# Kernel optimization log

Measured on AMD Instinct MI355X. Metric: run time of the kernel, lower is better.

## Reference

```python
import jax, jax.numpy as jnp
import numpy as np

B, S, D = 2, 1024, 768
H, HD = 12, 64
E, K, F = 8, 2, 3072
EPS = 1e-5


def _ln(x, g, b):
    mu = jnp.mean(x, -1, keepdims=True)
    var = jnp.mean(jnp.square(x - mu), -1, keepdims=True)
    return (x - mu) * jax.lax.rsqrt(var + EPS) * g + b


def setup_inputs() -> dict:
    key = jax.random.key(0)
    ks = jax.random.split(key, 12)
    s = lambda k, shape, sc: jax.random.normal(k, shape, jnp.float32) * sc
    return {
        "hidden_states": s(ks[0], (B, S, D), 1.0),
        "ln1_g": jnp.ones((D,), jnp.float32), "ln1_b": jnp.zeros((D,), jnp.float32),
        "w_attn": s(ks[1], (D, 3 * D), 0.02), "b_attn": jnp.zeros((3 * D,), jnp.float32),
        "w_attnproj": s(ks[2], (D, D), 0.02), "b_attnproj": jnp.zeros((D,), jnp.float32),
        "ln2_g": jnp.ones((D,), jnp.float32), "ln2_b": jnp.zeros((D,), jnp.float32),
        "w_router": s(ks[3], (E, D), 0.01),
        "w_fc": s(ks[4], (E, D, F), 0.02 / E), "b_fc": jnp.zeros((E, F), jnp.float32),
        "w_proj": s(ks[5], (E, F, D), 0.02 / E), "b_proj": jnp.zeros((E, D), jnp.float32),
    }


def reference(hidden_states, ln1_g, ln1_b, w_attn, b_attn, w_attnproj, b_attnproj,
              ln2_g, ln2_b, w_router, w_fc, b_fc, w_proj, b_proj):
    # --- attention sub-block (GPT-2 style, causal) ---
    residual = hidden_states
    x = _ln(hidden_states, ln1_g, ln1_b)
    qkv = x @ w_attn + b_attn                         # [B,S,3D]
    q, k, v = jnp.split(qkv, 3, axis=-1)
    def heads(t):
        return t.reshape(B, S, H, HD).transpose(0, 2, 1, 3)  # [B,H,S,HD]
    q, k, v = heads(q), heads(k), heads(v)
    scores = jnp.einsum("bhqd,bhkd->bhqk", q, k) / np.sqrt(HD).astype(np.float32)
    causal = jnp.tril(jnp.ones((S, S), bool))
    scores = jnp.where(causal, scores, jnp.finfo(scores.dtype).min)
    attn = jax.nn.softmax(scores, axis=-1)
    ctx = jnp.einsum("bhqk,bhkd->bhqd", attn, v)
    ctx = ctx.transpose(0, 2, 1, 3).reshape(B, S, D)
    attn_out = ctx @ w_attnproj + b_attnproj
    hs = attn_out + residual

    # --- MoE FFN sub-block ---
    residual = hs
    x2 = _ln(hs, ln2_g, ln2_b)
    logits = x2 @ w_router.T                          # [B,S,E]
    probs = jax.nn.softmax(logits, axis=-1)
    top_w, top_idx = jax.lax.top_k(probs, K)          # [B,S,K]
    top_w = top_w / jnp.sum(top_w, -1, keepdims=True)
    gates = jnp.sum(jax.nn.one_hot(top_idx, E, dtype=x2.dtype) * top_w[..., None], axis=2)  # [B,S,E]
    h = jax.nn.gelu(jnp.einsum("bsd,edf->bsef", x2, w_fc) + b_fc, approximate=False)
    y = jnp.einsum("bsef,efd->bsed", h, w_proj) + b_proj
    moe_out = jnp.einsum("bse,bsed->bsd", gates, y)
    return moe_out + residual
```

## Files before the change

### kernel.cpp

```cpp
#include <hip/hip_runtime.h>
#include <hip/hip_bf16.h>
#include <math.h>

#define NB 2
#define SEQ 1024
#define DM 768
#define NHEAD 12
#define HDIM 64
#define NEXP 8
#define FF 3072
#define NTOK (NB*SEQ)
#define TDIM (3*DM)
#define LNEPS 1e-5f
#define NSLOT (NTOK*2)

typedef __attribute__((ext_vector_type(8))) short v8s;
typedef __attribute__((ext_vector_type(4))) float v4f;

#define GLDS16(src, dst) \
    __builtin_amdgcn_global_load_lds((const __attribute__((address_space(1))) unsigned int*)(src), \
                                     (__attribute__((address_space(3))) unsigned int*)(dst), 16, 0, 0)

#define BARF() do { asm volatile("" ::: "memory"); __builtin_amdgcn_s_barrier(); asm volatile("" ::: "memory"); } while(0)
#define WAITV(n) asm volatile("s_waitcnt vmcnt(" #n ")" ::: "memory")

static __device__ __forceinline__ float bf2f(unsigned short u){
    return __uint_as_float(((unsigned)u) << 16);
}
static __device__ __forceinline__ unsigned short f2bf(float f){
    unsigned u = __float_as_uint(f);
    u += 0x7fffu + ((u >> 16) & 1u);
    return (unsigned short)(u >> 16);
}
static __device__ __forceinline__ float gelu_exact(float x){
    return 0.5f * x * (1.0f + erff(x * 0.70710678118654752440f));
}

__global__ __launch_bounds__(256) void tconv_kernel(const float* __restrict__ in,
                                                    unsigned short* __restrict__ out,
                                                    int R, int C){
    __shared__ float T[64][33];
    size_t base = (size_t)blockIdx.z * R * C;
    int c0 = blockIdx.x * 32, r0 = blockIdx.y * 64;
    int t = threadIdx.x;
    int row = t >> 2, cq = (t & 3) * 8;
    const float* ip = &in[base + (size_t)(r0 + row) * C + c0 + cq];
    float4 va = *(const float4*)ip;
    float4 vb = *(const float4*)(ip + 4);
    T[row][cq+0]=va.x; T[row][cq+1]=va.y; T[row][cq+2]=va.z; T[row][cq+3]=va.w;
    T[row][cq+4]=vb.x; T[row][cq+5]=vb.y; T[row][cq+6]=vb.z; T[row][cq+7]=vb.w;
    __syncthreads();
    int oc = t >> 3, or8 = (t & 7) * 8;
    unsigned short ov[8];
    #pragma unroll
    for (int i = 0; i < 8; i++) ov[i] = f2bf(T[or8 + i][oc]);
    *(v8s*)&out[base + (size_t)(c0 + oc) * R + r0 + or8] = *(const v8s*)ov;
}

__global__ __launch_bounds__(256) void ln_b(const float* __restrict__ in,
                                            const float* __restrict__ g,
                                            const float* __restrict__ b,
                                            unsigned short* __restrict__ outb){
    int t = blockIdx.x;
    const float* row = in + (size_t)t * DM;
    int tid = threadIdx.x;
    float v0 = row[tid], v1 = row[tid + 256], v2 = row[tid + 512];
    float s  = v0 + v1 + v2;
    float ss = v0*v0 + v1*v1 + v2*v2;
    for (int off = 32; off; off >>= 1){
        s  += __shfl_down(s, off);
        ss += __shfl_down(ss, off);
    }
    __shared__ float ls[4], lss[4];
    int wid = tid >> 6, lane = tid & 63;
    if (lane == 0){ ls[wid] = s; lss[wid] = ss; }
    __syncthreads();
    if (tid == 0){
        float a = ls[0] + ls[1] + ls[2] + ls[3];
        float c = lss[0] + lss[1] + lss[2] + lss[3];
        float mu = a / (float)DM;
        float var = c / (float)DM - mu * mu;
        ls[0] = mu; lss[0] = rsqrtf(var + LNEPS);
    }
    __syncthreads();
    float mu = ls[0], rs = lss[0];
    unsigned short* obrow = outb + (size_t)t * DM;
    obrow[tid]     = f2bf((v0 - mu) * rs * g[tid]       + b[tid]);
    obrow[tid+256] = f2bf((v1 - mu) * rs * g[tid + 256] + b[tid + 256]);
    obrow[tid+512] = f2bf((v2 - mu) * rs * g[tid + 512] + b[tid + 512]);
}

__global__ __launch_bounds__(256) void ln_router(const float* __restrict__ in,
                                                 const float* __restrict__ g,
                                                 const float* __restrict__ b,
                                                 const float* __restrict__ wr,
                                                 unsigned short* __restrict__ outb,
                                                 int* __restrict__ cnt,
                                                 int* __restrict__ expTok,
                                                 int* __restrict__ tokE,
                                                 int* __restrict__ tokPos,
                                                 float* __restrict__ tokGate){
    int t = blockIdx.x;
    const float* row = in + (size_t)t * DM;
    int tid = threadIdx.x;
    float v0 = row[tid], v1 = row[tid + 256], v2 = row[tid + 512];
    float s  = v0 + v1 + v2;
    float ss = v0*v0 + v1*v1 + v2*v2;
    for (int off = 32; off; off >>= 1){
        s  += __shfl_down(s, off);
        ss += __shfl_down(ss, off);
    }
    __shared__ float ls[4], lss[4];
    __shared__ float wsum[4][NEXP];
    int wid = tid >> 6, lane = tid & 63;
    if (lane == 0){ ls[wid] = s; lss[wid] = ss; }
    __syncthreads();
    if (tid == 0){
        float a = ls[0] + ls[1] + ls[2] + ls[3];
        float c = lss[0] + lss[1] + lss[2] + lss[3];
        float mu = a / (float)DM;
        float var = c / (float)DM - mu * mu;
        ls[0] = mu; lss[0] = rsqrtf(var + LNEPS);
    }
    __syncthreads();
    float mu = ls[0], rs = lss[0];
    float o0 = (v0 - mu) * rs * g[tid]       + b[tid];
    float o1 = (v1 - mu) * rs * g[tid + 256] + b[tid + 256];
    float o2 = (v2 - mu) * rs * g[tid + 512] + b[tid + 512];
    unsigned short* obrow = outb + (size_t)t * DM;
    obrow[tid] = f2bf(o0); obrow[tid+256] = f2bf(o1); obrow[tid+512] = f2bf(o2);
    float p[NEXP];
    #pragma unroll
    for (int e = 0; e < NEXP; e++)
        p[e] = o0*wr[e*DM + tid] + o1*wr[e*DM + tid + 256] + o2*wr[e*DM + tid + 512];
    #pragma unroll
    for (int e = 0; e < NEXP; e++)
        for (int off = 32; off; off >>= 1) p[e] += __shfl_down(p[e], off);
    if (lane == 0){
        #pragma unroll
        for (int e = 0; e < NEXP; e++) wsum[wid][e] = p[e];
    }
    __syncthreads();
    if (tid == 0){
        float lg[NEXP];
        #pragma unroll
        for (int e = 0; e < NEXP; e++)
            lg[e] = wsum[0][e] + wsum[1][e] + wsum[2][e] + wsum[3][e];
        int i0 = 0; float m0 = lg[0];
        #pragma unroll
        for (int e = 1; e < NEXP; e++) if (lg[e] > m0){ m0 = lg[e]; i0 = e; }
        int i1 = -1; float m1 = -INFINITY;
        #pragma unroll
        for (int e = 0; e < NEXP; e++) if (e != i0 && lg[e] > m1){ m1 = lg[e]; i1 = e; }
        float mx = fmaxf(m0, m1);
        float e0 = __expf(m0 - mx), e1 = __expf(m1 - mx);
        float inv = 1.0f / (e0 + e1);
        int p0 = atomicAdd(&cnt[i0], 1);
        int p1 = atomicAdd(&cnt[i1], 1);
        expTok[i0*NTOK + p0] = t;
        expTok[i1*NTOK + p1] = t;
        tokE[t*2]   = i0; tokE[t*2+1]   = i1;
        tokPos[t*2] = p0; tokPos[t*2+1] = p1;
        tokGate[t*2]   = e0 * inv;
        tokGate[t*2+1] = e1 * inv;
    }
}

__global__ __launch_bounds__(256) void mm_qkv(const unsigned short* __restrict__ Ab,
                                              const unsigned short* __restrict__ Bb,
                                              const float* __restrict__ bias,
                                              unsigned short* __restrict__ Qb,
                                              unsigned short* __restrict__ Kb,
                                              unsigned short* __restrict__ Vt){
    __shared__ __align__(16) unsigned short As[2][64*32];
    __shared__ __align__(16) unsigned short Bs[2][64*32];
    int bm = blockIdx.y * 64, bn = blockIdx.x * 64;
    int tid = threadIdx.x, wave = tid >> 6, lane = tid & 63;
    int quad = lane >> 4, l15 = lane & 15;
    int wm = wave >> 1, wn = wave & 1;
    int arow = tid >> 2, achunk = (tid & 3) * 8;
    const unsigned short* aS = Ab + (size_t)(bm + arow) * DM + achunk;
    const unsigned short* bS = Bb + (size_t)(bn + arow) * DM + achunk;
    v4f acc[2][2];
    #pragma unroll
    for (int i = 0; i < 2; i++)
        #pragma unroll
        for (int j = 0; j < 2; j++) acc[i][j] = (v4f){0.f,0.f,0.f,0.f};

#define QKV_STAGE(buf, kt) do { int kb = (kt)*32; \
    GLDS16(aS + kb, &As[buf][(wave*16)*32]); \
    GLDS16(bS + kb, &Bs[buf][(wave*16)*32]); \
} while(0)
#define QKV_COMP(buf) do { \
    v8s a[2], bfr[2]; \
    _Pragma("unroll") \
    for (int i = 0; i < 2; i++){ \
        a[i]   = *(const v8s*)&As[buf][(wm*32 + i*16 + l15)*32 + quad*8]; \
        bfr[i] = *(const v8s*)&Bs[buf][(wn*32 + i*16 + l15)*32 + quad*8]; \
    } \
    _Pragma("unroll") \
    for (int mi = 0; mi < 2; mi++) \
        _Pragma("unroll") \
        for (int ni = 0; ni < 2; ni++) \
            acc[mi][ni] = __builtin_amdgcn_mfma_f32_16x16x32_bf16(a[mi], bfr[ni], acc[mi][ni], 0, 0, 0); \
} while(0)

    const int NK = DM/32;
    QKV_STAGE(0, 0);
    #pragma unroll 1
    for (int kt = 0; kt < NK; kt++){
        if (NK - kt > 1){ QKV_STAGE((kt+1)&1, kt+1); WAITV(2); }
        else            { WAITV(0); }
        BARF();
        QKV_COMP(kt&1);
        BARF();
    }
    int btyp = bn / DM;
    #pragma unroll
    for (int ni = 0; ni < 2; ni++){
        int n = bn + wn*32 + ni*16 + l15;
        float bb = bias[n];
        int hd = n % DM; int h = hd >> 6; int d = hd & 63;
        #pragma unroll
        for (int mi = 0; mi < 2; mi++){
            int m = bm + wm*32 + mi*16 + quad*4;
            int b = m >> 10, sd = m & 1023;
            size_t bhbase = (size_t)(b*NHEAD + h);
            if (btyp == 0){
                #pragma unroll
                for (int r = 0; r < 4; r++)
                    Qb[(bhbase*SEQ + sd + r)*HDIM + d] = f2bf((acc[mi][ni][r] + bb) * 0.125f);
            } else if (btyp == 1){
                #pragma unroll
                for (int r = 0; r < 4; r++)
                    Kb[(bhbase*SEQ + sd + r)*HDIM + d] = f2bf(acc[mi][ni][r] + bb);
            } else {
                ushort4 o;
                o.x = f2bf(acc[mi][ni][0] + bb); o.y = f2bf(acc[mi][ni][1] + bb);
                o.z = f2bf(acc[mi][ni][2] + bb); o.w = f2bf(acc[mi][ni][3] + bb);
                *(ushort4*)&Vt[(bhbase*HDIM + d)*SEQ + sd] = o;
            }
        }
    }
}

__global__ __launch_bounds__(128) void fattn(const unsigned short* __restrict__ Qb,
                                             const unsigned short* __restrict__ Kb,
                                             const unsigned short* __restrict__ Vt,
                                             unsigned short* __restrict__ ctxb){
    int bh = blockIdx.x >> 5;
    int q0 = (31 - (blockIdx.x & 31)) * 32;
    int h = bh % NHEAD, b = bh / NHEAD;
    int wv = threadIdx.x >> 6;
    int lane = threadIdx.x & 63;
    int quad = lane >> 4, l15 = lane & 15;

    __shared__ __align__(16) unsigned short Plds[2][32*32];
    __shared__ __align__(16) v4f Oex[2][4][64];
    __shared__ float Mm[2][4][64];
    __shared__ float Lm[2][4][64];

    const unsigned short* qp = Qb + ((size_t)bh*SEQ + q0 + l15) * HDIM + quad*8;
    v8s qa00 = *(const v8s*)qp;
    v8s qa01 = *(const v8s*)(qp + 32);
    v8s qa10 = *(const v8s*)(qp + 16*HDIM);
    v8s qa11 = *(const v8s*)(qp + 16*HDIM + 32);

    v4f o[2][4];
    #pragma unroll
    for (int i = 0; i < 2; i++)
        #pragma unroll
        for (int j = 0; j < 4; j++) o[i][j] = (v4f){0.f,0.f,0.f,0.f};
    float mrow[2][4], lrow[2][4];
    #pragma unroll
    for (int i = 0; i < 2; i++)
        #pragma unroll
        for (int r = 0; r < 4; r++){ mrow[i][r] = -1e30f; lrow[i][r] = 0.f; }

    int nch = (q0 >> 5) + 1;
    int halfc = (nch + 1) >> 1;
    int ch0 = wv ? halfc : 0;
    int ch1 = wv ? nch : halfc;
    unsigned short* Pw = &Plds[wv][0];

    for (int ch = ch0; ch < ch1; ch++){
        int kt = ch * 32;
        const unsigned short* kp = Kb + ((size_t)bh*SEQ + kt + l15) * HDIM + quad*8;
        v8s k00 = *(const v8s*)kp;
        v8s k01 = *(const v8s*)(kp + 32);
        v8s k10 = *(const v8s*)(kp + 16*HDIM);
        v8s k11 = *(const v8s*)(kp + 16*HDIM + 32);
        v4f s00 = {0,0,0,0}, s01 = {0,0,0,0}, s10 = {0,0,0,0}, s11 = {0,0,0,0};
        s00 = __builtin_amdgcn_mfma_f32_16x16x32_bf16(qa00, k00, s00, 0, 0, 0);
        s00 = __builtin_amdgcn_mfma_f32_16x16x32_bf16(qa01, k01, s00, 0, 0, 0);
        s01 = __builtin_amdgcn_mfma_f32_16x16x32_bf16(qa00, k10, s01, 0, 0, 0);
        s01 = __builtin_amdgcn_mfma_f32_16x16x32_bf16(qa01, k11, s01, 0, 0, 0);
        s10 = __builtin_amdgcn_mfma_f32_16x16x32_bf16(qa10, k00, s10, 0, 0, 0);
        s10 = __builtin_amdgcn_mfma_f32_16x16x32_bf16(qa11, k01, s10, 0, 0, 0);
        s11 = __builtin_amdgcn_mfma_f32_16x16x32_bf16(qa10, k10, s11, 0, 0, 0);
        s11 = __builtin_amdgcn_mfma_f32_16x16x32_bf16(qa11, k11, s11, 0, 0, 0);

        int key0 = kt + l15, key1 = kt + 16 + l15;
        float alpha[2][4];
        #pragma unroll
        for (int mi = 0; mi < 2; mi++){
            #pragma unroll
            for (int r = 0; r < 4; r++){
                int qrow = q0 + mi*16 + quad*4 + r;
                float sv0 = mi ? s10[r] : s00[r];
                float sv1 = mi ? s11[r] : s01[r];
                float v0 = (key0 <= qrow) ? sv0 : -1e30f;
                float v1 = (key1 <= qrow) ? sv1 : -1e30f;
                float mx = fmaxf(v0, v1);
                mx = fmaxf(mx, __shfl_xor(mx, 1));
                mx = fmaxf(mx, __shfl_xor(mx, 2));
                mx = fmaxf(mx, __shfl_xor(mx, 4));
                mx = fmaxf(mx, __shfl_xor(mx, 8));
                float mn = fmaxf(mrow[mi][r], mx);
                alpha[mi][r] = __expf(mrow[mi][r] - mn);
                float p0 = __expf(v0 - mn);
                float p1 = __expf(v1 - mn);
                float ps = p0 + p1;
                ps += __shfl_xor(ps, 1);
                ps += __shfl_xor(ps, 2);
                ps += __shfl_xor(ps, 4);
                ps += __shfl_xor(ps, 8);
                lrow[mi][r] = lrow[mi][r] * alpha[mi][r] + ps;
                mrow[mi][r] = mn;
                Pw[(mi*16 + quad*4 + r)*32 + l15]      = f2bf(p0);
                Pw[(mi*16 + quad*4 + r)*32 + 16 + l15] = f2bf(p1);
            }
        }
        #pragma unroll
        for (int mi = 0; mi < 2; mi++)
            #pragma unroll
            for (int df = 0; df < 4; df++)
                #pragma unroll
                for (int r = 0; r < 4; r++)
                    o[mi][df][r] *= alpha[mi][r];
        v8s pa0 = *(const v8s*)&Pw[l15*32 + quad*8];
        v8s pa1 = *(const v8s*)&Pw[(16 + l15)*32 + quad*8];
        const unsigned short* vp = Vt + ((size_t)bh*HDIM + l15) * SEQ + kt + quad*8;
        #pragma unroll
        for (int df = 0; df < 4; df++){
            v8s vb = *(const v8s*)(vp + df*16*SEQ);
            o[0][df] = __builtin_amdgcn_mfma_f32_16x16x32_bf16(pa0, vb, o[0][df], 0, 0, 0);
            o[1][df] = __builtin_amdgcn_mfma_f32_16x16x32_bf16(pa1, vb, o[1][df], 0, 0, 0);
        }
    }

    int other = 1 - wv;
    #pragma unroll
    for (int df = 0; df < 4; df++) Oex[wv][df][lane] = o[other][df];
    #pragma unroll
    for (int r = 0; r < 4; r++){ Mm[wv][r][lane] = mrow[other][r]; Lm[wv][r][lane] = lrow[other][r]; }
    __syncthreads();
    v4f oth[4];
    #pragma unroll
    for (int df = 0; df < 4; df++) oth[df] = Oex[other][df][lane];
    #pragma unroll
    for (int r = 0; r < 4; r++){
        float mo = Mm[other][r][lane], lo_ = Lm[other][r][lane];
        float mm = mrow[wv][r], lm = lrow[wv][r];
        float M = fmaxf(mm, mo);
        float am = __expf(mm - M), ao = __expf(mo - M);
        float L = lm*am + lo_*ao;
        float inv = 1.0f / L;
        size_t orow = (size_t)(b*SEQ + q0 + wv*16 + quad*4 + r) * DM + h*HDIM;
        #pragma unroll
        for (int df = 0; df < 4; df++)
            ctxb[orow + df*16 + l15] = f2bf((o[wv][df][r]*am + oth[df][r]*ao) * inv);
    }
}

__global__ __launch_bounds__(256) void mm_attnproj(const unsigned short* __restrict__ Ab,
                                                   const unsigned short* __restrict__ Bb,
                                                   const float* __restrict__ bias,
                                                   const float* __restrict__ res,
                                                   float* __restrict__ C){
    __shared__ __align__(16) unsigned short As[4][64*32];
    __shared__ __align__(16) unsigned short Bs[4][64*32];
    int bm = blockIdx.y * 64, bn = blockIdx.x * 64;
    int tid = threadIdx.x, wave = tid >> 6, lane = tid & 63;
    int quad = lane >> 4, l15 = lane & 15;
    int wm = wave >> 1, wn = wave & 1;
    int lrow = lane >> 2, lchunk = (lane & 3) * 8;
    const unsigned short* aS = Ab + (size_t)(bm + wave*16 + lrow) * DM + lchunk;
    const unsigned short* bS = Bb + (size_t)(bn + wave*16 + lrow) * DM + lchunk;
    v4f acc[2][2];
    #pragma unroll
    for (int i = 0; i < 2; i++)
        #pragma unroll
        for (int j = 0; j < 2; j++) acc[i][j] = (v4f){0.f,0.f,0.f,0.f};

#define AP_STAGE(buf, kt) do { int kb = (kt)*32; \
    GLDS16(aS + kb, &As[buf][(wave*16)*32]); \
    GLDS16(bS + kb, &Bs[buf][(wave*16)*32]); \
} while(0)
#define AP_COMP(buf) do { \
    v8s a[2], bfr[2]; \
    _Pragma("unroll") \
    for (int i = 0; i < 2; i++){ \
        a[i]   = *(const v8s*)&As[buf][(wm*32 + i*16 + l15)*32 + quad*8]; \
        bfr[i] = *(const v8s*)&Bs[buf][(wn*32 + i*16 + l15)*32 + quad*8]; \
    } \
    _Pragma("unroll") \
    for (int mi = 0; mi < 2; mi++) \
        _Pragma("unroll") \
        for (int ni = 0; ni < 2; ni++) \
            acc[mi][ni] = __builtin_amdgcn_mfma_f32_16x16x32_bf16(a[mi], bfr[ni], acc[mi][ni], 0, 0, 0); \
} while(0)

    const int NK = DM/32;
    AP_STAGE(0, 0); AP_STAGE(1, 1); AP_STAGE(2, 2);
    #pragma unroll 1
    for (int kt = 0; kt < NK; kt++){
        int rem = NK - kt;
        if (rem > 3){ AP_STAGE((kt+3)&3, kt+3); WAITV(6); }
        else if (rem == 3){ WAITV(4); }
        else if (rem == 2){ WAITV(2); }
        else { WAITV(0); }
        BARF();
        AP_COMP(kt&3);
        BARF();
    }
    #pragma unroll
    for (int ni = 0; ni < 2; ni++){
        int n = bn + wn*32 + ni*16 + l15;
        float bb = bias[n];
        #pragma unroll
        for (int mi = 0; mi < 2; mi++){
            int m = bm + wm*32 + mi*16 + quad*4;
            #pragma unroll
            for (int r = 0; r < 4; r++)
                C[(size_t)(m + r) * DM + n] = acc[mi][ni][r] + bb + res[(size_t)(m + r) * DM + n];
        }
    }
}

__global__ __launch_bounds__(256) void mm_fc(const unsigned short* __restrict__ Xb,
                                             const unsigned short* __restrict__ Wb,
                                             const float* __restrict__ bfc,
                                             const int* __restrict__ expTok,
                                             const int* __restrict__ cnt,
                                             unsigned short* __restrict__ H){
    int bid = blockIdx.x;
    int e = bid & 7;
    int t2 = bid >> 3;
    int tile = t2 & 31;
    int bn = (t2 >> 5) * 128;
    int offe = 0, c = 0;
    #pragma unroll
    for (int j = 0; j < NEXP; j++){ int cj = cnt[j]; offe += (j < e) ? cj : 0; c = (j == e) ? cj : c; }
    int rows = c - tile * 64;
    if (rows <= 0) return;
    __shared__ __align__(16) unsigned short As[2][64*32];
    __shared__ __align__(16) unsigned short Bs[2][128*32];
    __shared__ int toks[64];
    int tid = threadIdx.x, wave = tid >> 6, lane = tid & 63;
    if (tid < 64){
        int idx = tile * 64 + tid;
        if (idx >= c) idx = c - 1;
        toks[tid] = expTok[e * NTOK + idx];
    }
    __syncthreads();
    int quad = lane >> 4, l15 = lane & 15;
    int wm = wave >> 1, wn = wave & 1;
    int lrow = lane >> 2;
    int pch = (((lane >> 3) & 3) ^ (lane & 3)) * 8;
    int tok0 = toks[wave*16 + lrow];
    const unsigned short* Be = Wb + (size_t)e * FF * DM;
    const unsigned short* aS  = Xb + (size_t)tok0 * DM + pch;
    const unsigned short* bS0 = Be + (size_t)(bn +      wave*16 + lrow) * DM + pch;
    const unsigned short* bS1 = Be + (size_t)(bn + 64 + wave*16 + lrow) * DM + pch;
    int q2 = (quad ^ ((l15 >> 1) & 3)) * 8;
    v4f acc[2][4];
    #pragma unroll
    for (int i = 0; i < 2; i++)
        #pragma unroll
        for (int j = 0; j < 4; j++) acc[i][j] = (v4f){0.f,0.f,0.f,0.f};

#define FC_STAGE(buf, kt) do { int kb = (kt)*32; \
    GLDS16(aS  + kb, &As[buf][(wave*16)*32]); \
    GLDS16(bS0 + kb, &Bs[buf][(     wave*16)*32]); \
    GLDS16(bS1 + kb, &Bs[buf][(64 + wave*16)*32]); \
} while(0)
#define FC_COMP(buf) do { \
    v8s a[2], bfr[4]; \
    _Pragma("unroll") \
    for (int i = 0; i < 2; i++) a[i] = *(const v8s*)&As[buf][(wm*32 + i*16 + l15)*32 + q2]; \
    _Pragma("unroll") \
    for (int i = 0; i < 4; i++) bfr[i] = *(const v8s*)&Bs[buf][(wn*64 + i*16 + l15)*32 + q2]; \
    _Pragma("unroll") \
    for (int mi = 0; mi < 2; mi++) \
        _Pragma("unroll") \
        for (int ni = 0; ni < 4; ni++) \
            acc[mi][ni] = __builtin_amdgcn_mfma_f32_16x16x32_bf16(a[mi], bfr[ni], acc[mi][ni], 0, 0, 0); \
} while(0)

    const int NK = DM/32;
    FC_STAGE(0, 0);
    #pragma unroll 1
    for (int kt = 0; kt < NK; kt++){
        if (NK - kt > 1){ FC_STAGE((kt+1)&1, kt+1); WAITV(3); }
        else            { WAITV(0); }
        BARF();
        FC_COMP(kt&1);
        BARF();
    }
    int slot0 = offe + tile * 64;
    #pragma unroll
    for (int ni = 0; ni < 4; ni++){
        int n = bn + wn*64 + ni*16 + l15;
        float bb = bfc[(size_t)e * FF + n];
        #pragma unroll
        for (int mi = 0; mi < 2; mi++){
            int ml = wm*32 + mi*16 + quad*4;
            #pragma unroll
            for (int r = 0; r < 4; r++)
                if (ml + r < rows)
                    H[(size_t)(slot0 + ml + r) * FF + n] = f2bf(gelu_exact(acc[mi][ni][r] + bb));
        }
    }
}

__global__ __launch_bounds__(256) void mm_proj(const unsigned short* __restrict__ H,
                                               const unsigned short* __restrict__ Wb,
                                               const int* __restrict__ cnt,
                                               float* __restrict__ Yp){
    int bid = blockIdx.x;
    int e = bid & 7;
    int t2 = bid >> 3;
    int tile = t2 & 31;
    int xx = t2 >> 5;
    int sk = xx & 1;
    int bn = (xx >> 1) * 64;
    int offe = 0, c = 0;
    #pragma unroll
    for (int j = 0; j < NEXP; j++){ int cj = cnt[j]; offe += (j < e) ? cj : 0; c = (j == e) ? cj : c; }
    int rows = c - tile * 64;
    if (rows <= 0) return;
    __shared__ __align__(16) unsigned short As[2][64*32];
    __shared__ __align__(16) unsigned short Bs[2][64*32];
    int tid = threadIdx.x, wave = tid >> 6, lane = tid & 63;
    int quad = lane >> 4, l15 = lane & 15;
    int wm = wave >> 1, wn = wave & 1;
    int slot0 = offe + tile * 64;
    int arow = tid >> 2;
    int pch = (((lane >> 3) & 3) ^ (lane & 3)) * 8;
    int arl = arow < rows ? arow : rows - 1;
    const unsigned short* Be = Wb + (size_t)e * DM * FF;
    const unsigned short* aS = H  + (size_t)(slot0 + arl) * FF + sk*1536 + pch;
    const unsigned short* bS = Be + (size_t)(bn + arow) * FF + sk*1536 + pch;
    int q2 = (quad ^ ((l15 >> 1) & 3)) * 8;
    v4f acc[2][2];
    #pragma unroll
    for (int i = 0; i < 2; i++)
        #pragma unroll
        for (int j = 0; j < 2; j++) acc[i][j] = (v4f){0.f,0.f,0.f,0.f};

#define PJ_STAGE(buf, kt) do { int kb = (kt)*32; \
    GLDS16(aS + kb, &As[buf][(wave*16)*32]); \
    GLDS16(bS + kb, &Bs[buf][(wave*16)*32]); \
} while(0)
#define PJ_COMP(buf) do { \
    v8s a[2], bfr[2]; \
    _Pragma("unroll") \
    for (int i = 0; i < 2; i++){ \
        a[i]   = *(const v8s*)&As[buf][(wm*32 + i*16 + l15)*32 + q2]; \
        bfr[i] = *(const v8s*)&Bs[buf][(wn*32 + i*16 + l15)*32 + q2]; \
    } \
    _Pragma("unroll") \
    for (int mi = 0; mi < 2; mi++) \
        _Pragma("unroll") \
        for (int ni = 0; ni < 2; ni++) \
            acc[mi][ni] = __builtin_amdgcn_mfma_f32_16x16x32_bf16(a[mi], bfr[ni], acc[mi][ni], 0, 0, 0); \
} while(0)

    const int NK = 1536/32;
    PJ_STAGE(0, 0);
    #pragma unroll 1
    for (int kt = 0; kt < NK; kt++){
        if (NK - kt > 1){ PJ_STAGE((kt+1)&1, kt+1); WAITV(2); }
        else            { WAITV(0); }
        BARF();
        PJ_COMP(kt&1);
        BARF();
    }
    float* Yo = Yp + (size_t)sk * NSLOT * DM;
    #pragma unroll
    for (int ni = 0; ni < 2; ni++){
        int n = bn + wn*32 + ni*16 + l15;
        #pragma unroll
        for (int mi = 0; mi < 2; mi++){
            int ml = wm*32 + mi*16 + quad*4;
            #pragma unroll
            for (int r = 0; r < 4; r++)
                if (ml + r < rows)
                    Yo[(size_t)(slot0 + ml + r) * DM + n] = acc[mi][ni][r];
        }
    }
}

__global__ __launch_bounds__(256) void combine_kernel(const float* __restrict__ hs,
                                                      const float* __restrict__ Yp,
                                                      const float* __restrict__ bproj,
                                                      const int* __restrict__ tokE,
                                                      const int* __restrict__ tokPos,
                                                      const float* __restrict__ tokGate,
                                                      const int* __restrict__ cnt,
                                                      float* __restrict__ out){
    int t = blockIdx.x;
    int e0 = tokE[t*2], e1 = tokE[t*2+1];
    int off0 = 0, off1 = 0;
    #pragma unroll
    for (int j = 0; j < NEXP; j++){
        int cj = cnt[j];
        off0 += (j < e0) ? cj : 0;
        off1 += (j < e1) ? cj : 0;
    }
    int s0 = off0 + tokPos[t*2];
    int s1 = off1 + tokPos[t*2+1];
    float g0 = tokGate[t*2], g1 = tokGate[t*2+1];
    const float* y0a = Yp + (size_t)s0 * DM;
    const float* y0b = Yp + (size_t)NSLOT * DM + (size_t)s0 * DM;
    const float* y1a = Yp + (size_t)s1 * DM;
    const float* y1b = Yp + (size_t)NSLOT * DM + (size_t)s1 * DM;
    const float* b0 = bproj + (size_t)e0 * DM;
    const float* b1 = bproj + (size_t)e1 * DM;
    const float* hr = hs + (size_t)t * DM;
    float* orow = out + (size_t)t * DM;
    for (int d = threadIdx.x; d < DM; d += 256){
        orow[d] = hr[d] + g0 * (y0a[d] + y0b[d] + b0[d]) + g1 * (y1a[d] + y1b[d] + b1[d]);
    }
}

extern "C" void kernel_launch(void* const* d_in, const int* in_sizes, int n_in,
                              void* d_out, int out_size, void* d_ws, size_t ws_size,
                              hipStream_t stream){
    (void)in_sizes; (void)n_in; (void)out_size; (void)ws_size;
    const float* hidden  = (const float*)d_in[0];
    const float* ln1_g   = (const float*)d_in[1];
    const float* ln1_b   = (const float*)d_in[2];
    const float* w_attn  = (const float*)d_in[3];
    const float* b_attn  = (const float*)d_in[4];
    const float* w_aproj = (const float*)d_in[5];
    const float* b_aproj = (const float*)d_in[6];
    const float* ln2_g   = (const float*)d_in[7];
    const float* ln2_b   = (const float*)d_in[8];
    const float* w_rout  = (const float*)d_in[9];
    const float* w_fc    = (const float*)d_in[10];
    const float* b_fc    = (const float*)d_in[11];
    const float* w_proj  = (const float*)d_in[12];
    const float* b_proj  = (const float*)d_in[13];
    float* out = (float*)d_out;

    char* ws = (char*)d_ws;
    float*          hs   = (float*)(ws + 0);
    unsigned short* xb   = (unsigned short*)(ws + 6291456);
    unsigned short* Qb   = (unsigned short*)(ws + 9437184);
    unsigned short* Kb   = (unsigned short*)(ws + 12582912);
    unsigned short* Vt   = (unsigned short*)(ws + 15728640);
    unsigned short* ctxb = (unsigned short*)(ws + 18874368);
    unsigned short* Wab  = (unsigned short*)(ws + 22020096);
    unsigned short* Wapb = (unsigned short*)(ws + 25559040);
    unsigned short* H    = (unsigned short*)(ws + 9437184);
    unsigned short* Wfcb = (unsigned short*)(ws + 34603008);
    unsigned short* Wprb = (unsigned short*)(ws + 72351744);
    float*          Yp   = (float*)(ws + 34603008);
    char* rt = ws + 110100480;
    int* cnt      = (int*)(rt + 0);
    int* expTok   = (int*)(rt + 128);
    int* tokE     = (int*)(rt + 128 + 65536);
    int* tokPos   = (int*)(rt + 128 + 81920);
    float* tokGate= (float*)(rt + 128 + 98304);

    hipMemsetAsync(cnt, 0, NEXP * sizeof(int), stream);

    tconv_kernel<<<dim3(TDIM/32, DM/64, 1), 256, 0, stream>>>(w_attn, Wab, DM, TDIM);
    tconv_kernel<<<dim3(DM/32, DM/64, 1), 256, 0, stream>>>(w_aproj, Wapb, DM, DM);
    tconv_kernel<<<dim3(FF/32, DM/64, NEXP), 256, 0, stream>>>(w_fc, Wfcb, DM, FF);
    tconv_kernel<<<dim3(DM/32, FF/64, NEXP), 256, 0, stream>>>(w_proj, Wprb, FF, DM);

    ln_b<<<NTOK, 256, 0, stream>>>(hidden, ln1_g, ln1_b, xb);
    mm_qkv<<<dim3(TDIM/64, NTOK/64), 256, 0, stream>>>(xb, Wab, b_attn, Qb, Kb, Vt);
    fattn<<<NB*NHEAD*32, 128, 0, stream>>>(Qb, Kb, Vt, ctxb);
    mm_attnproj<<<dim3(DM/64, NTOK/64), 256, 0, stream>>>(ctxb, Wapb, b_aproj, hidden, hs);
    ln_router<<<NTOK, 256, 0, stream>>>(hs, ln2_g, ln2_b, w_rout, xb,
                                        cnt, expTok, tokE, tokPos, tokGate);
    mm_fc<<<8 * (NTOK/64) * (FF/128), 256, 0, stream>>>(xb, Wfcb, b_fc, expTok, cnt, H);
    mm_proj<<<8 * (NTOK/64) * ((DM/64)*2), 256, 0, stream>>>(H, Wprb, cnt, Yp);
    combine_kernel<<<NTOK, 256, 0, stream>>>(hs, Yp, b_proj, tokE, tokPos, tokGate, cnt, out);
}
```

Before: 480.0 us.

## Drop split-K in expert down-projection and precompute expert offsets once

mm_proj no longer splits its K dimension of 3072 into two halves with separate partial output buffers. Each block now runs the full reduction and writes one Yp, so combine reads one partial per expert instead of two. A small offsets_kernel computes the expert prefix offsets once, replacing the per-block loop over counts in mm_fc, mm_proj and combine. This halves mm_proj's grid and doubles per-block K length, which may reduce parallelism and occupancy for the small, imbalanced expert tiles, and it adds one extra kernel launch.

Measured after the change: 496.8 us. 3.5% more time.

```diff
diff --git a/kernel.cpp b/kernel.cpp
--- a/kernel.cpp
+++ b/kernel.cpp
@@ -443,15 +443,14 @@
                                              const float* __restrict__ bfc,
                                              const int* __restrict__ expTok,
                                              const int* __restrict__ cnt,
+                                             const int* __restrict__ offE,
                                              unsigned short* __restrict__ H){
     int bid = blockIdx.x;
     int e = bid & 7;
     int t2 = bid >> 3;
     int tile = t2 & 31;
     int bn = (t2 >> 5) * 128;
-    int offe = 0, c = 0;
-    #pragma unroll
-    for (int j = 0; j < NEXP; j++){ int cj = cnt[j]; offe += (j < e) ? cj : 0; c = (j == e) ? cj : c; }
+    int c = cnt[e];
     int rows = c - tile * 64;
     if (rows <= 0) return;
     __shared__ __align__(16) unsigned short As[2][64*32];
@@ -508,7 +507,7 @@
         FC_COMP(kt&1);
         BARF();
     }
-    int slot0 = offe + tile * 64;
+    int slot0 = offE[e] + tile * 64;
     #pragma unroll
     for (int ni = 0; ni < 4; ni++){
         int n = bn + wn*64 + ni*16 + l15;
@@ -527,17 +526,14 @@
 __global__ __launch_bounds__(256) void mm_proj(const unsigned short* __restrict__ H,
                                                const unsigned short* __restrict__ Wb,
                                                const int* __restrict__ cnt,
+                                               const int* __restrict__ offE,
                                                float* __restrict__ Yp){
     int bid = blockIdx.x;
     int e = bid & 7;
     int t2 = bid >> 3;
     int tile = t2 & 31;
-    int xx = t2 >> 5;
-    int sk = xx & 1;
-    int bn = (xx >> 1) * 64;
-    int offe = 0, c = 0;
-    #pragma unroll
-    for (int j = 0; j < NEXP; j++){ int cj = cnt[j]; offe += (j < e) ? cj : 0; c = (j == e) ? cj : c; }
+    int bn = (t2 >> 5) * 64;
+    int c = cnt[e];
     int rows = c - tile * 64;
     if (rows <= 0) return;
     __shared__ __align__(16) unsigned short As[2][64*32];
@@ -545,13 +541,13 @@
     int tid = threadIdx.x, wave = tid >> 6, lane = tid & 63;
     int quad = lane >> 4, l15 = lane & 15;
     int wm = wave >> 1, wn = wave & 1;
-    int slot0 = offe + tile * 64;
+    int slot0 = offE[e] + tile * 64;
     int arow = tid >> 2;
     int pch = (((lane >> 3) & 3) ^ (lane & 3)) * 8;
     int arl = arow < rows ? arow : rows - 1;
     const unsigned short* Be = Wb + (size_t)e * DM * FF;
-    const unsigned short* aS = H  + (size_t)(slot0 + arl) * FF + sk*1536 + pch;
-    const unsigned short* bS = Be + (size_t)(bn + arow) * FF + sk*1536 + pch;
+    const unsigned short* aS = H  + (size_t)(slot0 + arl) * FF + pch;
+    const unsigned short* bS = Be + (size_t)(bn + arow) * FF + pch;
     int q2 = (quad ^ ((l15 >> 1) & 3)) * 8;
     v4f acc[2][2];
     #pragma unroll
@@ -577,7 +573,7 @@
             acc[mi][ni] = __builtin_amdgcn_mfma_f32_16x16x32_bf16(a[mi], bfr[ni], acc[mi][ni], 0, 0, 0); \
 } while(0)
 
-    const int NK = 1536/32;
+    const int NK = FF/32;
     PJ_STAGE(0, 0);
     #pragma unroll 1
     for (int kt = 0; kt < NK; kt++){
@@ -587,7 +583,6 @@
         PJ_COMP(kt&1);
         BARF();
     }
-    float* Yo = Yp + (size_t)sk * NSLOT * DM;
     #pragma unroll
     for (int ni = 0; ni < 2; ni++){
         int n = bn + wn*32 + ni*16 + l15;
@@ -597,8 +592,15 @@
             #pragma unroll
             for (int r = 0; r < 4; r++)
                 if (ml + r < rows)
-                    Yo[(size_t)(slot0 + ml + r) * DM + n] = acc[mi][ni][r];
+                    Yp[(size_t)(slot0 + ml + r) * DM + n] = acc[mi][ni][r];
         }
+    }
+}
+
+__global__ void offsets_kernel(const int* __restrict__ cnt, int* __restrict__ offE){
+    if (threadIdx.x == 0 && blockIdx.x == 0){
+        int a = 0;
+        for (int e = 0; e < NEXP; e++){ offE[e] = a; a += cnt[e]; }
     }
 }
 
@@ -608,30 +610,21 @@
                                                       const int* __restrict__ tokE,
                                                       const int* __restrict__ tokPos,
                                                       const float* __restrict__ tokGate,
-                                                      const int* __restrict__ cnt,
+                                                      const int* __restrict__ offE,
                                                       float* __restrict__ out){
     int t = blockIdx.x;
     int e0 = tokE[t*2], e1 = tokE[t*2+1];
-    int off0 = 0, off1 = 0;
-    #pragma unroll
-    for (int j = 0; j < NEXP; j++){
-        int cj = cnt[j];
-        off0 += (j < e0) ? cj : 0;
-        off1 += (j < e1) ? cj : 0;
-    }
-    int s0 = off0 + tokPos[t*2];
-    int s1 = off1 + tokPos[t*2+1];
+    int s0 = offE[e0] + tokPos[t*2];
+    int s1 = offE[e1] + tokPos[t*2+1];
     float g0 = tokGate[t*2], g1 = tokGate[t*2+1];
-    const float* y0a = Yp + (size_t)s0 * DM;
-    const float* y0b = Yp + (size_t)NSLOT * DM + (size_t)s0 * DM;
-    const float* y1a = Yp + (size_t)s1 * DM;
-    const float* y1b = Yp + (size_t)NSLOT * DM + (size_t)s1 * DM;
+    const float* y0 = Yp + (size_t)s0 * DM;
+    const float* y1 = Yp + (size_t)s1 * DM;
     const float* b0 = bproj + (size_t)e0 * DM;
     const float* b1 = bproj + (size_t)e1 * DM;
     const float* hr = hs + (size_t)t * DM;
     float* orow = out + (size_t)t * DM;
     for (int d = threadIdx.x; d < DM; d += 256){
-        orow[d] = hr[d] + g0 * (y0a[d] + y0b[d] + b0[d]) + g1 * (y1a[d] + y1b[d] + b1[d]);
+        orow[d] = hr[d] + g0 * (y0[d] + b0[d]) + g1 * (y1[d] + b1[d]);
     }
 }
 
@@ -670,6 +663,7 @@
     float*          Yp   = (float*)(ws + 34603008);
     char* rt = ws + 110100480;
     int* cnt      = (int*)(rt + 0);
+    int* offE     = (int*)(rt + 64);
     int* expTok   = (int*)(rt + 128);
     int* tokE     = (int*)(rt + 128 + 65536);
     int* tokPos   = (int*)(rt + 128 + 81920);
@@ -688,7 +682,8 @@
     mm_attnproj<<<dim3(DM/64, NTOK/64), 256, 0, stream>>>(ctxb, Wapb, b_aproj, hidden, hs);
     ln_router<<<NTOK, 256, 0, stream>>>(hs, ln2_g, ln2_b, w_rout, xb,
                                         cnt, expTok, tokE, tokPos, tokGate);
-    mm_fc<<<8 * (NTOK/64) * (FF/128), 256, 0, stream>>>(xb, Wfcb, b_fc, expTok, cnt, H);
-    mm_proj<<<8 * (NTOK/64) * ((DM/64)*2), 256, 0, stream>>>(H, Wprb, cnt, Yp);
-    combine_kernel<<<NTOK, 256, 0, stream>>>(hs, Yp, b_proj, tokE, tokPos, tokGate, cnt, out);
-}
+    offsets_kernel<<<1, 64, 0, stream>>>(cnt, offE);
+    mm_fc<<<8 * (NTOK/64) * (FF/128), 256, 0, stream>>>(xb, Wfcb, b_fc, expTok, cnt, offE, H);
+    mm_proj<<<8 * (NTOK/64) * (DM/64), 256, 0, stream>>>(H, Wprb, cnt, offE, Yp);
+    combine_kernel<<<NTOK, 256, 0, stream>>>(hs, Yp, b_proj, tokE, tokPos, tokGate, offE, out);
+}
```
